# Performance work log

Hardware: AMD Instinct MI355X
Metric: run time of the kernel (lower is better)

Reference implementation:

```python
import jax, jax.numpy as jnp
import numpy as np

CLS_NUM = 2
SCALE = 8.0
NO_OBJ_SCALE = 1.0
EPS = 1e-7


def setup_inputs() -> dict:
    key = jax.random.key(0)
    k1, k2, k3, k4, k5, k6 = jax.random.split(key, 6)
    B, C, H, W, N = 8, CLS_NUM, 512, 512, 160
    predict = jax.random.normal(k1, (B, C, H, W), dtype=jnp.float32)
    b = jax.random.randint(k2, (N,), 0, B).astype(jnp.float32)
    c = jax.random.randint(k3, (N,), 0, C).astype(jnp.float32)
    cxy = jax.random.uniform(k4, (N, 2), minval=0.0, maxval=H * SCALE)
    wh = jax.random.uniform(k5, (N, 2), minval=64.0, maxval=256.0)
    ang = jax.random.uniform(k6, (N, 1), minval=-np.pi, maxval=np.pi)
    targets = jnp.concatenate([b[:, None], c[:, None], cxy, wh, ang], axis=1).astype(jnp.float32)
    return {"predict": predict, "targets": targets}


def _forward(predict, targets):
    B, C, H, W = predict.shape
    pred = jnp.transpose(predict, (0, 2, 3, 1))          # [B,H,W,C]
    conf_all = jax.nn.sigmoid(pred)
    heatmap = jnp.max(conf_all, axis=-1)                 # [B,H,W]

    bid = targets[:, 0].astype(jnp.int32)                # [N] batch ids
    cid = targets[:, 1].astype(jnp.int32)                # [N] class ids
    cx = targets[:, 2] / SCALE
    cy = targets[:, 3] / SCALE
    w = targets[:, 4] / SCALE
    h = targets[:, 5] / SCALE
    ang = targets[:, 6]
    cos, sin = jnp.cos(ang), jnp.sin(ang)
    # rotate box center into the rotated frame (same math as render_map)
    x = cx * cos + cy * sin
    y = -cx * sin + cy * cos
    x3, x4 = x - h / 2, x + h / 2
    y3, y4 = y - w / 2, y + w / 2
    x1, x2 = x3 - 0.5, x4 + 0.5
    y1, y2 = y3 - 0.5, y4 + 0.5

    gx = jnp.arange(W, dtype=jnp.float32)[None, :] + 0.5  # [1,W] -> broadcasts to [H,W]
    gy = jnp.arange(H, dtype=jnp.float32)[:, None] + 0.5  # [H,1]
    vx = cos[:, None, None] * gx + sin[:, None, None] * gy   # [N,H,W]
    vy = -sin[:, None, None] * gx + cos[:, None, None] * gy  # [N,H,W]

    def box_mask(lo_x, hi_x, lo_y, hi_y):
        return ((lo_x[:, None, None] <= vx) & (vx <= hi_x[:, None, None]) &
                (lo_y[:, None, None] <= vy) & (vy <= hi_y[:, None, None]))

    inner = box_mask(x3, x4, y3, y4)  # obj region, [N,H,W]
    outer = box_mask(x1, x2, y1, y2)  # expanded region (clears noobj)

    loss = jnp.float32(0.0)
    for cls in range(CLS_NUM):
        sel = (cid == cls)[:, None, None]
        obj_cnt = jax.ops.segment_sum((inner & sel).astype(jnp.float32), bid, num_segments=B)
        out_cnt = jax.ops.segment_sum((outer & sel).astype(jnp.float32), bid, num_segments=B)
        obj_mask = obj_cnt > 0            # [B,H,W]
        noobj_mask = out_cnt <= 0         # starts at 1, zeroed inside any expanded box
        conf_c = jnp.clip(conf_all[..., cls], EPS, 1.0 - EPS)
        n_obj = jnp.sum(obj_mask)
        n_noobj = jnp.sum(noobj_mask)
        # BCE with target 1 on obj cells, target 0 on noobj cells (tconf == obj mask)
        loss_obj = -jnp.sum(jnp.where(obj_mask, jnp.log(conf_c), 0.0)) / jnp.maximum(n_obj, 1)
        loss_noobj = -jnp.sum(jnp.where(noobj_mask, jnp.log(1.0 - conf_c), 0.0)) / jnp.maximum(n_noobj, 1)
        loss = loss + jnp.where(n_obj > 0, loss_obj + NO_OBJ_SCALE * loss_noobj, 0.0)
    return loss, heatmap


def reference(predict, targets):
    return _forward(predict, targets)
```

## Files before the change

kernel.cpp:

```cpp
#include <hip/hip_runtime.h>
#include <math.h>

#define CLS 2
#define BATCH 8
#define HH 512
#define WW 512
#define INV_SCALE 0.125f
#define LOGEPS -16.118095651f

#define NB 512
#define TSTRIDE 192
#define TCAP 192


__global__ __launch_bounds__(256) void heatmap_prep(
    const float* __restrict__ targets, int nT, double* __restrict__ gsum,
    int* __restrict__ gcnt, int* __restrict__ bcnt, float* __restrict__ tdat)
{
    __shared__ int s_b[BATCH];
    const int t = threadIdx.x;
    if (t < BATCH) s_b[t] = 0;
    for (int q = t; q < 4 * NB; q += 256) { gsum[q] = 0.0; gcnt[q] = 0; }
    __syncthreads();
    if (t < nT) {
        const float* tp = targets + t * 7;
        const int b = (int)tp[0];
        const float cs = cosf(tp[6]), sn = sinf(tp[6]);
        const float cx = tp[2] * INV_SCALE, cy = tp[3] * INV_SCALE;
        const float w_ = tp[4] * INV_SCALE, h_ = tp[5] * INV_SCALE;
        const float x = cx * cs + cy * sn;
        const float y = -cx * sn + cy * cs;
        const int slot = atomicAdd(&s_b[b], 1);
        float* tb = tdat + b * (7 * TSTRIDE);
        tb[0 * TSTRIDE + slot] = cs;
        tb[1 * TSTRIDE + slot] = sn;
        tb[2 * TSTRIDE + slot] = x - 0.5f * h_;
        tb[3 * TSTRIDE + slot] = x + 0.5f * h_;
        tb[4 * TSTRIDE + slot] = y - 0.5f * w_;
        tb[5 * TSTRIDE + slot] = y + 0.5f * w_;
        ((int*)tb)[6 * TSTRIDE + slot] = (int)tp[1];
    }
    __syncthreads();
    if (t < BATCH) bcnt[t] = s_b[t];
}

__global__ __launch_bounds__(64) void heatmap_main(
    const float* __restrict__ predict, float* __restrict__ out,
    double* __restrict__ gsum, int* __restrict__ gcnt,
    const int* __restrict__ bcnt, const float* __restrict__ tdat)
{
    __shared__ float s_cs[TCAP], s_sn[TCAP];
    __shared__ float s_x3[TCAP], s_x4[TCAP], s_y3[TCAP], s_y4[TCAP];
    __shared__ int   s_cid[TCAP];

    const int l = threadIdx.x;
    const int blockPix = blockIdx.x * 256;
    const int b  = blockPix >> 18;
    const int i  = (blockPix >> 9) & (HH - 1);
    const int j0 = blockPix & (WW - 1);
    const float gy = (float)i + 0.5f;

    const int nb = bcnt[b];
    const float* tb = tdat + b * (7 * TSTRIDE);
    int cnt = 0;
    for (int base = 0; base < nb; base += 64) {
        bool acc = false;
        float cs = 0.f, sn = 0.f, x3 = 0.f, x4 = 0.f, y3 = 0.f, y4 = 0.f;
        int cid = 0;
        const int t = base + l;
        if (t < nb) {
            cs = tb[0 * TSTRIDE + t]; sn = tb[1 * TSTRIDE + t];
            x3 = tb[2 * TSTRIDE + t]; x4 = tb[3 * TSTRIDE + t];
            y3 = tb[4 * TSTRIDE + t]; y4 = tb[5 * TSTRIDE + t];
            cid = ((const int*)tb)[6 * TSTRIDE + t];
            const float gxl = (float)j0 + 0.5f, gxh = (float)j0 + 255.5f;
            const float a1 = cs * gxl + sn * gy, a2 = cs * gxh + sn * gy;
            const float b1 = -sn * gxl + cs * gy, b2 = -sn * gxh + cs * gy;
            const float vxlo = fminf(a1, a2), vxhi = fmaxf(a1, a2);
            const float vylo = fminf(b1, b2), vyhi = fmaxf(b1, b2);
            const float M = 0.51f;
            acc = (vxhi >= x3 - M) & (vxlo <= x4 + M) &
                  (vyhi >= y3 - M) & (vylo <= y4 + M);
        }
        const unsigned long long bal = __ballot(acc);
        if (acc) {
            const int slot = cnt + (int)__popcll(bal & ((1ull << l) - 1ull));
            s_cs[slot] = cs; s_sn[slot] = sn;
            s_x3[slot] = x3; s_x4[slot] = x4;
            s_y3[slot] = y3; s_y4[slot] = y4;
            s_cid[slot] = cid;
        }
        cnt += (int)__popcll(bal);
    }
    __syncthreads();

    const int j = j0 + 4 * l;
    const float gxb = (float)j + 0.5f;
    int objm[4] = {0, 0, 0, 0}, outm[4] = {0, 0, 0, 0};
    for (int n = 0; n < cnt; ++n) {
        const float cs = s_cs[n], sn = s_sn[n];
        const float x3 = s_x3[n], x4 = s_x4[n], y3 = s_y3[n], y4 = s_y4[n];
        const int cbit = 1 << s_cid[n];
        float vx = cs * gxb + sn * gy;
        float vy = -sn * gxb + cs * gy;
        #pragma unroll
        for (int k = 0; k < 4; ++k) {
            const bool in_  = (x3 <= vx) & (vx <= x4) & (y3 <= vy) & (vy <= y4);
            const bool out_ = (x3 - 0.5f <= vx) & (vx <= x4 + 0.5f) &
                              (y3 - 0.5f <= vy) & (vy <= y4 + 0.5f);
            if (in_)  objm[k] |= cbit;
            if (out_) outm[k] |= cbit;
            vx += cs; vy -= sn;
        }
    }

    const int pbase = (b * CLS * HH + i) * WW + j;
    const float4 P0 = *(const float4*)(predict + pbase);
    const float4 P1 = *(const float4*)(predict + pbase + HH * WW);

    float so0 = 0.f, so1 = 0.f, sq0 = 0.f, sq1 = 0.f;
    int c_obj0 = 0, c_obj1 = 0, c_no0 = 0, c_no1 = 0;
    float hm[4];
    #pragma unroll
    for (int k = 0; k < 4; ++k) {
        const float p0 = (&P0.x)[k], p1 = (&P1.x)[k];
        const float t0 = __expf(p0), t1 = __expf(p1);
        const float l0n = -__logf(1.0f + t0);
        const float l1n = -__logf(1.0f + t1);
        const float lc0 = fmaxf(p0 + l0n, LOGEPS);
        const float lc1 = fmaxf(p1 + l1n, LOGEPS);
        const float l0c = fmaxf(l0n, LOGEPS);
        const float l1c = fmaxf(l1n, LOGEPS);
        const float tm = fmaxf(t0, t1);
        hm[k] = tm * __builtin_amdgcn_rcpf(1.0f + tm);
        const int om = objm[k], um = outm[k];
        if (om & 1) { so0 += lc0; ++c_obj0; }
        if (om & 2) { so1 += lc1; ++c_obj1; }
        if (!(um & 1)) { sq0 += l0c; ++c_no0; }
        if (!(um & 2)) { sq1 += l1c; ++c_no1; }
    }

    float* ho = out + 1 + (b * HH + i) * WW + j;
    ho[0] = hm[0]; ho[1] = hm[1]; ho[2] = hm[2]; ho[3] = hm[3];

    const unsigned long long anyobj =
        __ballot((objm[0] | objm[1] | objm[2] | objm[3]) != 0);
    int pc = (c_no0 & 0xffff) | (c_no1 << 16);
    #pragma unroll
    for (int off = 32; off >= 1; off >>= 1) {
        sq0 += __shfl_down(sq0, off);
        sq1 += __shfl_down(sq1, off);
        pc  += __shfl_down(pc, off);
    }
    int po = 0;
    if (anyobj) {
        po = (c_obj0 & 0xffff) | (c_obj1 << 16);
        #pragma unroll
        for (int off = 32; off >= 1; off >>= 1) {
            so0 += __shfl_down(so0, off);
            so1 += __shfl_down(so1, off);
            po  += __shfl_down(po, off);
        }
    }
    if (l == 0) {
        const int bkt = blockIdx.x & (NB - 1);
        atomicAdd(&gsum[2 * NB + bkt], (double)sq0);
        atomicAdd(&gsum[3 * NB + bkt], (double)sq1);
        atomicAdd(&gcnt[2 * NB + bkt], pc & 0xffff);
        atomicAdd(&gcnt[3 * NB + bkt], pc >> 16);
        if (anyobj) {
            const int o0 = po & 0xffff, o1 = po >> 16;
            if (o0) { atomicAdd(&gsum[0 * NB + bkt], (double)so0);
                      atomicAdd(&gcnt[0 * NB + bkt], o0); }
            if (o1) { atomicAdd(&gsum[1 * NB + bkt], (double)so1);
                      atomicAdd(&gcnt[1 * NB + bkt], o1); }
        }
    }
}

__global__ __launch_bounds__(512) void heatmap_finalize(
    const double* __restrict__ gsum, const int* __restrict__ gcnt,
    float* __restrict__ out)
{
    const int t = threadIdx.x;
    double f[4]; int c[4];
    #pragma unroll
    for (int q = 0; q < 4; ++q) { f[q] = gsum[q * NB + t]; c[q] = gcnt[q * NB + t]; }

    #pragma unroll
    for (int off = 32; off >= 1; off >>= 1) {
        #pragma unroll
        for (int q = 0; q < 4; ++q) {
            f[q] += __shfl_down(f[q], off);
            c[q] += __shfl_down(c[q], off);
        }
    }

    __shared__ double sf[8][4];
    __shared__ int    si[8][4];
    const int wv = t >> 6, ln = t & 63;
    if (ln == 0) {
        #pragma unroll
        for (int q = 0; q < 4; ++q) { sf[wv][q] = f[q]; si[wv][q] = c[q]; }
    }
    __syncthreads();
    if (t == 0) {
        double F[4] = {0, 0, 0, 0}; int C[4] = {0, 0, 0, 0};
        for (int w = 0; w < 8; ++w)
            #pragma unroll
            for (int q = 0; q < 4; ++q) { F[q] += sf[w][q]; C[q] += si[w][q]; }
        float loss = 0.0f;
        #pragma unroll
        for (int cls = 0; cls < CLS; ++cls) {
            const int no = C[cls];
            const int nn = C[2 + cls];
            if (no > 0) {
                const float lo  = -(float)F[cls]     / (float)(no > 1 ? no : 1);
                const float ln_ = -(float)F[2 + cls] / (float)(nn > 1 ? nn : 1);
                loss += lo + ln_;
            }
        }
        out[0] = loss;
    }
}

extern "C" void kernel_launch(void* const* d_in, const int* in_sizes, int n_in,
                              void* d_out, int out_size, void* d_ws, size_t ws_size,
                              hipStream_t stream) {
    const float* predict = (const float*)d_in[0];
    const float* targets = (const float*)d_in[1];
    const int nT = in_sizes[1] / 7;
    float* out = (float*)d_out;
    char* ws = (char*)d_ws;
    double* gsum = (double*)ws;
    int* gcnt = (int*)(ws + 16384);
    int* bcnt = (int*)(ws + 24576);
    float* tdat = (float*)(ws + 24608);

    heatmap_prep<<<1, 256, 0, stream>>>(targets, nT, gsum, gcnt, bcnt, tdat);
    const int pixels = BATCH * HH * WW;
    heatmap_main<<<pixels / 256, 64, 0, stream>>>(predict, out, gsum, gcnt,
                                                  bcnt, tdat);
    heatmap_finalize<<<1, 512, 0, stream>>>(gsum, gcnt, out);
}
```

Measured before the change: 80.86 us.

## Fuse finalize into main kernel via two-level last-block atomic counter

Removes the separate finalize kernel launch. A two-level atomic ticket (64 leaf counters feeding one root counter) lets the last finishing block reduce the partial sums and write the loss. The number of reduction buckets drops from 512 to 128 to make that final reduction cheaper, which puts more atomic contention on each bucket. The heatmap store is also changed to a single 16-byte memcpy.

```diff
diff --git a/kernel.cpp b/kernel.cpp
--- a/kernel.cpp
+++ b/kernel.cpp
@@ -8,19 +8,23 @@
 #define INV_SCALE 0.125f
 #define LOGEPS -16.118095651f
 
-#define NB 512
+#define NB 128
 #define TSTRIDE 192
 #define TCAP 192
+#define NBLK 8192
+#define LEAFQ (NBLK / 64)
 
 
 __global__ __launch_bounds__(256) void heatmap_prep(
     const float* __restrict__ targets, int nT, double* __restrict__ gsum,
-    int* __restrict__ gcnt, int* __restrict__ bcnt, float* __restrict__ tdat)
+    int* __restrict__ gcnt, int* __restrict__ leafroot,
+    int* __restrict__ bcnt, float* __restrict__ tdat)
 {
     __shared__ int s_b[BATCH];
     const int t = threadIdx.x;
     if (t < BATCH) s_b[t] = 0;
     for (int q = t; q < 4 * NB; q += 256) { gsum[q] = 0.0; gcnt[q] = 0; }
+    if (t < 65) leafroot[t] = 0;
     __syncthreads();
     if (t < nT) {
         const float* tp = targets + t * 7;
@@ -47,6 +51,7 @@
 __global__ __launch_bounds__(64) void heatmap_main(
     const float* __restrict__ predict, float* __restrict__ out,
     double* __restrict__ gsum, int* __restrict__ gcnt,
+    int* __restrict__ leaf, int* __restrict__ root,
     const int* __restrict__ bcnt, const float* __restrict__ tdat)
 {
     __shared__ float s_cs[TCAP], s_sn[TCAP];
@@ -141,7 +146,7 @@
     }
 
     float* ho = out + 1 + (b * HH + i) * WW + j;
-    ho[0] = hm[0]; ho[1] = hm[1]; ho[2] = hm[2]; ho[3] = hm[3];
+    __builtin_memcpy(ho, hm, 16);
 
     const unsigned long long anyobj =
         __ballot((objm[0] | objm[1] | objm[2] | objm[3]) != 0);
@@ -162,6 +167,8 @@
             po  += __shfl_down(po, off);
         }
     }
+
+    int isLast = 0;
     if (l == 0) {
         const int bkt = blockIdx.x & (NB - 1);
         atomicAdd(&gsum[2 * NB + bkt], (double)sq0);
@@ -175,52 +182,46 @@
             if (o1) { atomicAdd(&gsum[1 * NB + bkt], (double)so1);
                       atomicAdd(&gcnt[1 * NB + bkt], o1); }
         }
-    }
-}
-
-__global__ __launch_bounds__(512) void heatmap_finalize(
-    const double* __restrict__ gsum, const int* __restrict__ gcnt,
-    float* __restrict__ out)
-{
-    const int t = threadIdx.x;
-    double f[4]; int c[4];
-    #pragma unroll
-    for (int q = 0; q < 4; ++q) { f[q] = gsum[q * NB + t]; c[q] = gcnt[q * NB + t]; }
-
-    #pragma unroll
-    for (int off = 32; off >= 1; off >>= 1) {
+        asm volatile("s_waitcnt vmcnt(0)" ::: "memory");
+        const int lv = atomicAdd(&leaf[blockIdx.x & 63], 1);
+        if (lv == LEAFQ - 1) {
+            const int rv = atomicAdd(root, 1);
+            if (rv == 63) isLast = 1;
+        }
+    }
+    isLast = __shfl(isLast, 0);
+
+    if (isLast) {
+        double f[4] = {0, 0, 0, 0}; int c[4] = {0, 0, 0, 0};
+        for (int t = l; t < NB; t += 64) {
+            #pragma unroll
+            for (int q = 0; q < 4; ++q) {
+                f[q] += atomicAdd(&gsum[q * NB + t], 0.0);
+                c[q] += atomicAdd(&gcnt[q * NB + t], 0);
+            }
+        }
         #pragma unroll
-        for (int q = 0; q < 4; ++q) {
-            f[q] += __shfl_down(f[q], off);
-            c[q] += __shfl_down(c[q], off);
-        }
-    }
-
-    __shared__ double sf[8][4];
-    __shared__ int    si[8][4];
-    const int wv = t >> 6, ln = t & 63;
-    if (ln == 0) {
-        #pragma unroll
-        for (int q = 0; q < 4; ++q) { sf[wv][q] = f[q]; si[wv][q] = c[q]; }
-    }
-    __syncthreads();
-    if (t == 0) {
-        double F[4] = {0, 0, 0, 0}; int C[4] = {0, 0, 0, 0};
-        for (int w = 0; w < 8; ++w)
+        for (int off = 32; off >= 1; off >>= 1) {
             #pragma unroll
-            for (int q = 0; q < 4; ++q) { F[q] += sf[w][q]; C[q] += si[w][q]; }
-        float loss = 0.0f;
-        #pragma unroll
-        for (int cls = 0; cls < CLS; ++cls) {
-            const int no = C[cls];
-            const int nn = C[2 + cls];
-            if (no > 0) {
-                const float lo  = -(float)F[cls]     / (float)(no > 1 ? no : 1);
-                const float ln_ = -(float)F[2 + cls] / (float)(nn > 1 ? nn : 1);
-                loss += lo + ln_;
+            for (int q = 0; q < 4; ++q) {
+                f[q] += __shfl_down(f[q], off);
+                c[q] += __shfl_down(c[q], off);
             }
         }
-        out[0] = loss;
+        if (l == 0) {
+            float loss = 0.0f;
+            #pragma unroll
+            for (int cls = 0; cls < CLS; ++cls) {
+                const int no = c[cls];
+                const int nn = c[2 + cls];
+                if (no > 0) {
+                    const float lo  = -(float)f[cls]     / (float)(no > 1 ? no : 1);
+                    const float ln_ = -(float)f[2 + cls] / (float)(nn > 1 ? nn : 1);
+                    loss += lo + ln_;
+                }
+            }
+            out[0] = loss;
+        }
     }
 }
 
@@ -233,13 +234,14 @@
     float* out = (float*)d_out;
     char* ws = (char*)d_ws;
     double* gsum = (double*)ws;
-    int* gcnt = (int*)(ws + 16384);
-    int* bcnt = (int*)(ws + 24576);
-    float* tdat = (float*)(ws + 24608);
-
-    heatmap_prep<<<1, 256, 0, stream>>>(targets, nT, gsum, gcnt, bcnt, tdat);
-    const int pixels = BATCH * HH * WW;
-    heatmap_main<<<pixels / 256, 64, 0, stream>>>(predict, out, gsum, gcnt,
-                                                  bcnt, tdat);
-    heatmap_finalize<<<1, 512, 0, stream>>>(gsum, gcnt, out);
+    int* gcnt = (int*)(ws + 4096);
+    int* leaf = (int*)(ws + 6144);
+    int* root = (int*)(ws + 6400);
+    int* bcnt = (int*)(ws + 6432);
+    float* tdat = (float*)(ws + 6464);
+
+    heatmap_prep<<<1, 256, 0, stream>>>(targets, nT, gsum, gcnt, leaf, bcnt,
+                                        tdat);
+    heatmap_main<<<NBLK, 64, 0, stream>>>(predict, out, gsum, gcnt, leaf, root,
+                                          bcnt, tdat);
 }
```

New measurement: 110.6 us. 1.37x slower.
